# Kernel tuning notes

Measured on AMD Instinct MI355X. Metric: run time of the kernel, lower is better.

The kernel has to match this reference:

```python
import jax, jax.numpy as jnp
import numpy as np

NEG = jnp.float32(-1e30)  # finite stand-in for -inf (grad-safe)
B, T_MAX, K_MAX = 64, 2000, 400
BLANK_LOGPROB = -1.0


def setup_inputs() -> dict:
    key = jax.random.key(0)
    k1, k2, k3, k4 = jax.random.split(key, 4)
    attn = jax.random.normal(k1, (B, 1, T_MAX, K_MAX), jnp.float32)
    attn_logprob = jax.random.normal(k2, (B, 1, T_MAX, K_MAX), jnp.float32)
    in_lens = jax.random.randint(k3, (B,), K_MAX // 2, K_MAX + 1)   # text lengths in [200,400]
    out_lens = jax.random.randint(k4, (B,), T_MAX // 2, T_MAX + 1)  # mel lengths in [1000,2000]
    return {"attn": attn, "in_lens": in_lens, "out_lens": out_lens, "attn_logprob": attn_logprob}


def ctc_alignment_loss(attn_logprob, in_lens, out_lens):
    # attn_logprob: [B, 1, T, K]; targets for sample b are arange(1, in_lens[b]+1), blank=0.
    Bn, _, T, K = attn_logprob.shape
    C = K + 1
    # pad blank class (index 0) with constant blank_logprob, as in F.pad(..., value=blank_logprob)
    lp = jnp.concatenate(
        [jnp.full((Bn, T, 1), BLANK_LOGPROB, attn_logprob.dtype), attn_logprob[:, 0]], axis=-1
    )  # [B, T, C]
    # per-sample log_softmax restricted to classes [0 .. in_len] (original slices :key_len+1 first)
    cls_mask = jnp.arange(C)[None, :] <= in_lens[:, None]          # [B, C]
    lp = jnp.where(cls_mask[:, None, :], lp, NEG)
    lp = jax.nn.log_softmax(lp, axis=-1)                            # [B, T, C]

    # extended CTC state sequence: blank, 1, blank, 2, ..., K, blank  (S = 2K+1)
    S = 2 * K + 1
    s = jnp.arange(S)
    ext = jnp.where(s % 2 == 1, (s + 1) // 2, 0)                    # labels per state
    lp_ext = jnp.take(lp, ext, axis=-1)                             # [B, T, S]
    allow2 = (s % 2 == 1) & (s >= 2)                                # skip-transition allowed (targets have no repeats)

    alpha0 = jnp.full((Bn, S), NEG, lp.dtype)
    alpha0 = alpha0.at[:, 0].set(lp_ext[:, 0, 0]).at[:, 1].set(lp_ext[:, 0, 1])

    def step(alpha, inputs):
        lp_t, t = inputs  # lp_t: [B, S]
        a1 = jnp.concatenate([jnp.full((Bn, 1), NEG, alpha.dtype), alpha[:, :-1]], axis=1)
        a2 = jnp.concatenate([jnp.full((Bn, 2), NEG, alpha.dtype), alpha[:, :-2]], axis=1)
        a2 = jnp.where(allow2[None, :], a2, NEG)
        new = lp_t + jnp.logaddexp(jnp.logaddexp(alpha, a1), a2)
        alpha = jnp.where((t < out_lens)[:, None], new, alpha)      # freeze past each sample's query_len
        return alpha, None

    xs = (lp_ext.transpose(1, 0, 2)[1:], jnp.arange(1, T))
    alpha, _ = jax.lax.scan(step, alpha0, xs)

    idx_last = 2 * in_lens                                           # final blank state per sample
    a_last = jnp.take_along_axis(alpha, idx_last[:, None], axis=1)[:, 0]
    a_prev = jnp.take_along_axis(alpha, (idx_last - 1)[:, None], axis=1)[:, 0]
    ll = jnp.logaddexp(a_last, a_prev)
    # nn.CTCLoss(reduction='mean') with batch 1: divide by target length; zero_infinity -> 0
    loss = jnp.where(ll > 0.5 * NEG, -ll / in_lens.astype(lp.dtype), jnp.zeros((), lp.dtype))
    return jnp.mean(loss)


def reference(attn, in_lens, out_lens, attn_logprob):
    # attn is accepted but unused, matching the original forward signature
    return ctc_alignment_loss(attn_logprob, in_lens, out_lens)
```

## Files before the change

### kernel.cpp

```cpp
#include <hip/hip_runtime.h>
#include <cmath>


#define T_MAXN 2000
#define K_MAXN 400

typedef uint32_t uint4v __attribute__((ext_vector_type(4)));

#define G_BYTES   ((size_t)64 * T_MAXN * K_MAXN * 2)
#define LSE_OFF   G_BYTES
#define LSE_BYTES ((size_t)64 * T_MAXN * 4)
#define ZERO_OFF  (LSE_OFF + LSE_BYTES)
#define LOSS_OFF  (ZERO_OFF + 4096)
#define WS_NEED   (LOSS_OFF + 64 * 4)

__device__ __forceinline__ float dpp_wave_shr1(float x)
{
    int r = __builtin_amdgcn_update_dpp(0, (int)__float_as_uint(x),
                                        0x138 , 0xF, 0xF, true);
    return __uint_as_float((uint32_t)r);
}

template <int CTRL>
__device__ __forceinline__ float dpp_mov(float x)
{
    int r = __builtin_amdgcn_update_dpp(0, (int)__float_as_uint(x),
                                        CTRL, 0xF, 0xF, true);
    return __uint_as_float((uint32_t)r);
}

__global__ __launch_bounds__(256)
void prep_kernel(const float* __restrict__ ap_all,
                 const int* __restrict__ in_lens,
                 const int* __restrict__ out_lens,
                 float* __restrict__ lse_out,
                 _Float16* __restrict__ g_out,
                 float* __restrict__ zerobuf)
{
    const int b    = blockIdx.y;
    const int L    = in_lens[b];
    const int Tn   = out_lens[b];
    const int lane = threadIdx.x & 63;
    const int wid  = blockIdx.x * (blockDim.x >> 6) + (threadIdx.x >> 6);
    const int nw   = gridDim.x * (blockDim.x >> 6);

    if (b == 0 && wid == 0) {
        for (int i = lane; i < 1024; i += 64) zerobuf[i] = 0.0f;
    }

    const float* base = ap_all + (size_t)b * (T_MAXN * K_MAXN);
    _Float16*    gb   = g_out  + (size_t)b * (T_MAXN * K_MAXN);
    const int c0 = lane * 8;
    const int cb = (c0 < 392) ? c0 : 392;

    for (int t = wid; t < Tn; t += nw) {
        const float4* p = reinterpret_cast<const float4*>(base + (size_t)t * K_MAXN + cb);
        float4 x0 = p[0], x1 = p[1];
        float v[8] = {x0.x, x0.y, x0.z, x0.w, x1.x, x1.y, x1.z, x1.w};
        float m = -1.0f;
        #pragma unroll
        for (int j = 0; j < 8; ++j) {
            v[j] = (c0 + j < L) ? v[j] : -1e30f;
            m = fmaxf(m, v[j]);
        }
        #pragma unroll
        for (int off = 32; off; off >>= 1) m = fmaxf(m, __shfl_xor(m, off));
        float s = (lane == 0) ? __expf(-1.0f - m) : 0.0f;
        #pragma unroll
        for (int j = 0; j < 8; ++j) s += __expf(v[j] - m);
        #pragma unroll
        for (int off = 32; off; off >>= 1) s += __shfl_xor(s, off);
        if (lane == 0) lse_out[b * T_MAXN + t] = m + __logf(s);

        _Float16 h[8];
        #pragma unroll
        for (int j = 0; j < 8; ++j) h[j] = (_Float16)__expf(v[j] + 1.0f);
        if (c0 < K_MAXN)
            *reinterpret_cast<uint4v*>(gb + (size_t)t * K_MAXN + c0) =
                *reinterpret_cast<const uint4v*>(h);
    }
}

__global__ __launch_bounds__(256, 1)
void ctc_scan4w_kernel(const char* wsro,
                       const int* __restrict__ in_lens,
                       const int* __restrict__ out_lens,
                       float* loss_out)
{
    __shared__ float afin[1024];
    __shared__ float halo_sh[4][32];
    __shared__ float wmax_sh[4];

    const int b    = blockIdx.x;
    const int tid  = threadIdx.x;
    const int wid  = tid >> 6;
    const int lane = tid & 63;
    const int L    = in_lens[b];
    const int Tn   = out_lens[b];
    const uint32_t goff = (uint32_t)b * (uint32_t)(T_MAXN * K_MAXN * 2);
    const float* lse = (const float*)(wsro + LSE_OFF) + b * T_MAXN;

    const int col0 = 112 * wid - 16 + 2 * lane;
    uint32_t off, inc;
    if (col0 >= 0 && col0 < K_MAXN) { off = goff + (uint32_t)(col0 * 2) + 800u; inc = 3200u; }
    else                            { off = (uint32_t)ZERO_OFF;                 inc = 0u;    }

    float sl = 0.0f;
    if (wid == 0) {
        for (int t = lane; t < Tn; t += 64) sl += lse[t];
        #pragma unroll
        for (int o = 32; o; o >>= 1) sl += __shfl_xor(sl, o);
    }

    float a0=0.0f, a1=0.0f, a2=0.0f, a3=0.0f;
    if (wid == 0 && lane == 8) {
        a0 = 1.0f;
        a1 = (float)*reinterpret_cast<const _Float16*>(wsro + goff);
    }
    int   E  = 0;
    float t1 = 0.0f;

    #define LOADG4(QA, QB, QC, QD) do { \
        asm volatile("global_load_dword %0, %1, %2 offset:0"    : "=v"(QA) : "v"(off), "s"(wsro)); \
        asm volatile("global_load_dword %0, %1, %2 offset:800"  : "=v"(QB) : "v"(off), "s"(wsro)); \
        asm volatile("global_load_dword %0, %1, %2 offset:1600" : "=v"(QC) : "v"(off), "s"(wsro)); \
        asm volatile("global_load_dword %0, %1, %2 offset:2400" : "=v"(QD) : "v"(off), "s"(wsro)); \
        off += inc; \
    } while (0)

    #define WAITG12 do { \
        asm volatile("s_waitcnt vmcnt(12)" ::: "memory"); \
        __builtin_amdgcn_sched_barrier(0); \
    } while (0)

    #define FMIXLO(DST, SRC, O) \
        asm("v_fma_mix_f32 %0, %1, %2, 0 op_sel:[0,0,0] op_sel_hi:[1,0,0]" \
            : "=v"(DST) : "v"(SRC), "v"(O))
    #define FMIXHI(DST, SRC, O) \
        asm("v_fma_mix_f32 %0, %1, %2, 0 op_sel:[1,0,0] op_sel_hi:[1,0,0]" \
            : "=v"(DST) : "v"(SRC), "v"(O))

    #define STEPF(Q) do { \
        const float e0 = a0 + t1; \
        const float e1 = a2 + a1; \
        const float o0 = a1 + e0; \
        const float o1 = a3 + e1; \
        a0 = e0; a2 = e1; \
        FMIXLO(a1, (Q), o0); \
        FMIXHI(a3, (Q), o1); \
        t1 = dpp_wave_shr1(a3); \
    } while (0)

    #define BARR do { \
        asm volatile("s_waitcnt lgkmcnt(0)" ::: "memory"); \
        __builtin_amdgcn_s_barrier(); \
        asm volatile("" ::: "memory"); \
    } while (0)

    #define EXCHANGE do { \
        float mx = fmaxf(fmaxf(a0, a1), fmaxf(a2, a3)); \
        mx = fmaxf(mx, dpp_mov<0x111>(mx)); \
        mx = fmaxf(mx, dpp_mov<0x112>(mx)); \
        mx = fmaxf(mx, dpp_mov<0x114>(mx)); \
        mx = fmaxf(mx, dpp_mov<0x118>(mx)); \
        mx = fmaxf(mx, dpp_mov<0x142>(mx)); \
        mx = fmaxf(mx, dpp_mov<0x143>(mx)); \
        if (lane == 63) wmax_sh[wid] = mx; \
        if (lane >= 56) { \
            float4 bv; bv.x = a0; bv.y = a1; bv.z = a2; bv.w = a3; \
            *reinterpret_cast<float4*>(&halo_sh[wid][(lane - 56) * 4]) = bv; \
        } \
        BARR; \
        float bm = fmaxf(fmaxf(wmax_sh[0], wmax_sh[1]), fmaxf(wmax_sh[2], wmax_sh[3])); \
        int e = (int)((__float_as_uint(bm) >> 23) & 0xFF) - 127; \
        E += e; \
        const float sc = __uint_as_float((uint32_t)(127 - e) << 23);   \
        if (wid > 0 && lane < 8) { \
            float4 hv = *reinterpret_cast<const float4*>(&halo_sh[wid - 1][lane * 4]); \
            a0 = hv.x; a1 = hv.y; a2 = hv.z; a3 = hv.w; \
        } \
        a0 *= sc; a1 *= sc; a2 *= sc; a3 *= sc; \
        t1 = dpp_wave_shr1(a3); \
        BARR; \
    } while (0)

    uint32_t q0,q1,q2,q3,q4,q5,q6,q7,q8,q9,q10,q11,q12,q13,q14,q15;
    LOADG4(q0,q1,q2,q3); LOADG4(q4,q5,q6,q7);
    LOADG4(q8,q9,q10,q11); LOADG4(q12,q13,q14,q15);

    int t = 1;
    while (t + 15 < Tn) {
        WAITG12; STEPF(q0);  STEPF(q1);  STEPF(q2);  STEPF(q3);  LOADG4(q0,q1,q2,q3);
        WAITG12; STEPF(q4);  STEPF(q5);  STEPF(q6);  STEPF(q7);  LOADG4(q4,q5,q6,q7);
        WAITG12; STEPF(q8);  STEPF(q9);  STEPF(q10); STEPF(q11); LOADG4(q8,q9,q10,q11);
        WAITG12; STEPF(q12); STEPF(q13); STEPF(q14); STEPF(q15); LOADG4(q12,q13,q14,q15);
        EXCHANGE;
        t += 16;
    }
    asm volatile("s_waitcnt vmcnt(0)" ::: "memory");
    __builtin_amdgcn_sched_barrier(0);
    {
        const int r = Tn - t;
        if (r > 0)  STEPF(q0);
        if (r > 1)  STEPF(q1);
        if (r > 2)  STEPF(q2);
        if (r > 3)  STEPF(q3);
        if (r > 4)  STEPF(q4);
        if (r > 5)  STEPF(q5);
        if (r > 6)  STEPF(q6);
        if (r > 7)  STEPF(q7);
        if (r > 8)  STEPF(q8);
        if (r > 9)  STEPF(q9);
        if (r > 10) STEPF(q10);
        if (r > 11) STEPF(q11);
        if (r > 12) STEPF(q12);
        if (r > 13) STEPF(q13);
        if (r > 14) STEPF(q14);
    }

    if (lane >= 8) {
        const int gidx = 224 * wid - 32 + 4 * lane;
        afin[gidx]     = a0;
        afin[gidx + 1] = a1;
        afin[gidx + 2] = a2;
        afin[gidx + 3] = a3;
    }
    __syncthreads();
    if (tid == 0) {
        float tot = afin[2 * L] + afin[2 * L - 1];
        float lossb = 0.0f;
        if (tot > 0.0f) {
            double ll = log((double)tot)
                      + (double)E * 0.69314718055994530942
                      + (double)(-(double)Tn - (double)sl);
            lossb = (float)(-ll / (double)L);
        }
        loss_out[b] = lossb;
    }
    #undef STEPF
    #undef FMIXLO
    #undef FMIXHI
    #undef LOADG4
    #undef WAITG12
    #undef BARR
    #undef EXCHANGE
}

__global__ __launch_bounds__(256)
void lse_kernel(const float* __restrict__ ap_all,
                const int* __restrict__ in_lens,
                float* __restrict__ lse_out)
{
    const int lane = threadIdx.x & 63;
    const int wglob = blockIdx.x * (blockDim.x >> 6) + (threadIdx.x >> 6);
    const int nwav = gridDim.x * (blockDim.x >> 6);
    const int nrows = 64 * T_MAXN;

    for (int row = wglob; row < nrows; row += nwav) {
        const int b = row / T_MAXN;
        const int L = in_lens[b];
        const float* rp = ap_all + (size_t)row * K_MAXN;
        const int c0 = lane * 8;
        const int cb = (c0 < 392) ? c0 : 392;
        const float4* p = reinterpret_cast<const float4*>(rp + cb);
        float4 x0 = p[0], x1 = p[1];
        float v[8] = {x0.x, x0.y, x0.z, x0.w, x1.x, x1.y, x1.z, x1.w};
        float m = -1.0f;
        #pragma unroll
        for (int j = 0; j < 8; ++j) {
            v[j] = (c0 + j < L) ? v[j] : -1e30f;
            m = fmaxf(m, v[j]);
        }
        #pragma unroll
        for (int off = 32; off; off >>= 1) m = fmaxf(m, __shfl_xor(m, off));
        float s = (lane == 0) ? __expf(-1.0f - m) : 0.0f;
        #pragma unroll
        for (int j = 0; j < 8; ++j) s += __expf(v[j] - m);
        #pragma unroll
        for (int off = 32; off; off >>= 1) s += __shfl_xor(s, off);
        if (lane == 0) lse_out[row] = m + __logf(s);
    }
}

__global__ __launch_bounds__(64)
void ctc_scan_kernel(const float* __restrict__ ap_all,
                     const int* __restrict__ in_lens,
                     const int* __restrict__ out_lens,
                     const float* __restrict__ lse_all,
                     float* __restrict__ loss_out)
{
    __shared__ float afin[1024];

    const int b    = blockIdx.x;
    const int lane = threadIdx.x;
    const int L    = in_lens[b];
    const int Tn   = out_lens[b];
    const float* ap  = ap_all + (size_t)b * (T_MAXN * K_MAXN);
    const float* lse = lse_all + b * T_MAXN;

    const float LOG2E = 1.4426950408889634f;
    const int c0 = lane * 8;
    const int cb = (c0 < 392) ? c0 : 392;
    const float* rbase = ap + cb;
    float fa0,fa1,fa2,fa3,fa4,fa5,fa6,fa7;
    float fb0,fb1,fb2,fb3,fb4,fb5,fb6,fb7;
    #define MASKC(J, FA, FB) do { bool ok = (c0 + (J)) < L; \
        FA = ok ? LOG2E : 0.0f; FB = ok ? LOG2E : -1000.0f; } while (0)
    MASKC(0,fa0,fb0); MASKC(1,fa1,fb1); MASKC(2,fa2,fb2); MASKC(3,fa3,fb3);
    MASKC(4,fa4,fb4); MASKC(5,fa5,fb5); MASKC(6,fa6,fb6); MASKC(7,fa7,fb7);
    #undef MASKC

    float4 p0a,p0b,p1a,p1b,p2a,p2b,p3a,p3b;
    #define LOADROW(PA, PB, T) do { \
        const float4* _p = reinterpret_cast<const float4*>(rbase + (size_t)(T) * K_MAXN); \
        PA = _p[0]; PB = _p[1]; } while (0)
    LOADROW(p0a,p0b,1); LOADROW(p1a,p1b,2); LOADROW(p2a,p2b,3); LOADROW(p3a,p3b,4);

    float sl = 0.0f;
    for (int t = lane; t < Tn; t += 64) sl += lse[t];
    #pragma unroll
    for (int off = 32; off; off >>= 1) sl += __shfl_xor(sl, off);

    float x00 = ap[0];
    float a0=0,a1=0,a2=0,a3=0,a4=0,a5=0,a6=0,a7=0;
    float a8=0,a9=0,a10=0,a11=0,a12=0,a13=0,a14=0,a15=0;
    if (lane == 0) {
        a0 = 1.0f;
        a1 = __builtin_amdgcn_exp2f(fmaf(x00, LOG2E, LOG2E));
    }
    int E = 0;

    #define STEP(A0, A1) do { \
        float t1 = __shfl_up(a15, 1); \
        t1 = lane ? t1 : 0.0f; \
        const float f0 = __builtin_amdgcn_exp2f(fmaf((A0).x, fa0, fb0)); \
        const float f1 = __builtin_amdgcn_exp2f(fmaf((A0).y, fa1, fb1)); \
        const float f2 = __builtin_amdgcn_exp2f(fmaf((A0).z, fa2, fb2)); \
        const float f3 = __builtin_amdgcn_exp2f(fmaf((A0).w, fa3, fb3)); \
        const float f4 = __builtin_amdgcn_exp2f(fmaf((A1).x, fa4, fb4)); \
        const float f5 = __builtin_amdgcn_exp2f(fmaf((A1).y, fa5, fb5)); \
        const float f6 = __builtin_amdgcn_exp2f(fmaf((A1).z, fa6, fb6)); \
        const float f7 = __builtin_amdgcn_exp2f(fmaf((A1).w, fa7, fb7)); \
        const float e0 = a0 + t1,   e1 = a2 + a1,   e2 = a4 + a3,   e3 = a6 + a5; \
        const float e4 = a8 + a7,   e5 = a10 + a9,  e6 = a12 + a11, e7 = a14 + a13; \
        const float o0 = a1 + e0,   o1 = a3 + e1,   o2 = a5 + e2,   o3 = a7 + e3; \
        const float o4 = a9 + e4,   o5 = a11 + e5,  o6 = a13 + e6,  o7 = a15 + e7; \
        a0 = e0; a2 = e1; a4 = e2; a6 = e3; a8 = e4; a10 = e5; a12 = e6; a14 = e7; \
        a1 = f0*o0; a3 = f1*o1; a5 = f2*o2; a7 = f3*o3; \
        a9 = f4*o4; a11 = f5*o5; a13 = f6*o6; a15 = f7*o7; \
    } while (0)

    #define RESCALE do { \
        float mx = fmaxf(fmaxf(fmaxf(fmaxf(a0,a1),fmaxf(a2,a3)),fmaxf(fmaxf(a4,a5),fmaxf(a6,a7))), \
                         fmaxf(fmaxf(fmaxf(a8,a9),fmaxf(a10,a11)),fmaxf(fmaxf(a12,a13),fmaxf(a14,a15)))); \
        _Pragma("unroll") \
        for (int off = 32; off; off >>= 1) mx = fmaxf(mx, __shfl_xor(mx, off)); \
        int e = (int)((__float_as_uint(mx) >> 23) & 0xFF) - 127; \
        if (e != 0) { \
            E += e; \
            a0 = ldexpf(a0,-e);  a1 = ldexpf(a1,-e);  a2 = ldexpf(a2,-e);  a3 = ldexpf(a3,-e); \
            a4 = ldexpf(a4,-e);  a5 = ldexpf(a5,-e);  a6 = ldexpf(a6,-e);  a7 = ldexpf(a7,-e); \
            a8 = ldexpf(a8,-e);  a9 = ldexpf(a9,-e);  a10= ldexpf(a10,-e); a11= ldexpf(a11,-e); \
            a12= ldexpf(a12,-e); a13= ldexpf(a13,-e); a14= ldexpf(a14,-e); a15= ldexpf(a15,-e); \
        } \
    } while (0)

    int t = 1;
    while (t + 3 < Tn) {
        int tl;
        STEP(p0a,p0b); tl = (t+4 < T_MAXN) ? t+4 : T_MAXN-1; LOADROW(p0a,p0b,tl);
        STEP(p1a,p1b); tl = (t+5 < T_MAXN) ? t+5 : T_MAXN-1; LOADROW(p1a,p1b,tl);
        STEP(p2a,p2b); tl = (t+6 < T_MAXN) ? t+6 : T_MAXN-1; LOADROW(p2a,p2b,tl);
        STEP(p3a,p3b); tl = (t+7 < T_MAXN) ? t+7 : T_MAXN-1; LOADROW(p3a,p3b,tl);
        if ((t & 7) == 5) RESCALE;
        t += 4;
    }
    if (t < Tn) { STEP(p0a,p0b); ++t; }
    if (t < Tn) { STEP(p1a,p1b); ++t; }
    if (t < Tn) { STEP(p2a,p2b); ++t; }

    afin[16*lane+0]=a0;  afin[16*lane+1]=a1;  afin[16*lane+2]=a2;  afin[16*lane+3]=a3;
    afin[16*lane+4]=a4;  afin[16*lane+5]=a5;  afin[16*lane+6]=a6;  afin[16*lane+7]=a7;
    afin[16*lane+8]=a8;  afin[16*lane+9]=a9;  afin[16*lane+10]=a10; afin[16*lane+11]=a11;
    afin[16*lane+12]=a12; afin[16*lane+13]=a13; afin[16*lane+14]=a14; afin[16*lane+15]=a15;
    __syncthreads();
    if (lane == 0) {
        float tot = afin[2*L] + afin[2*L-1];
        float lossb = 0.0f;
        if (tot > 0.0f) {
            double ll = log((double)tot)
                      + (double)E * 0.69314718055994530942
                      + (double)(-(double)Tn - (double)sl);
            lossb = (float)(-ll / (double)L);
        }
        loss_out[b] = lossb;
    }
    #undef STEP
    #undef RESCALE
    #undef LOADROW
}

__global__ void mean_kernel(const float* __restrict__ loss, float* __restrict__ out)
{
    float v = loss[threadIdx.x];
    #pragma unroll
    for (int off = 32; off; off >>= 1) v += __shfl_xor(v, off);
    if (threadIdx.x == 0) out[0] = v * (1.0f / 64.0f);
}

extern "C" void kernel_launch(void* const* d_in, const int* in_sizes, int n_in,
                              void* d_out, int out_size, void* d_ws, size_t ws_size,
                              hipStream_t stream)
{
    const int*   in_lens  = (const int*)d_in[1];
    const int*   out_lens = (const int*)d_in[2];
    const float* ap       = (const float*)d_in[3];
    float*       out      = (float*)d_out;

    if (ws_size >= WS_NEED) {
        char*     wsb     = (char*)d_ws;
        _Float16* g       = (_Float16*)wsb;
        float*    lse_ws  = (float*)(wsb + LSE_OFF);
        float*    zb      = (float*)(wsb + ZERO_OFF);
        float*    loss_ws = (float*)(wsb + LOSS_OFF);
        hipLaunchKernelGGL(prep_kernel, dim3(32, 64), dim3(256), 0, stream,
                           ap, in_lens, out_lens, lse_ws, g, zb);
        hipLaunchKernelGGL(ctc_scan4w_kernel, dim3(64), dim3(256), 0, stream,
                           (const char*)wsb, in_lens, out_lens, loss_ws);
        hipLaunchKernelGGL(mean_kernel, dim3(1), dim3(64), 0, stream, loss_ws, out);
    } else {
        float* lse_ws  = (float*)d_ws;
        float* loss_ws = (float*)((char*)d_ws + (size_t)64 * T_MAXN * 4);
        hipLaunchKernelGGL(lse_kernel, dim3(512), dim3(256), 0, stream,
                           ap, in_lens, lse_ws);
        hipLaunchKernelGGL(ctc_scan_kernel, dim3(64), dim3(64), 0, stream,
                           ap, in_lens, out_lens, lse_ws, loss_ws);
        hipLaunchKernelGGL(mean_kernel, dim3(1), dim3(64), 0, stream, loss_ws, out);
    }
}
```

Before: 120.1 us.

## Double-buffer halo exchange to drop second barrier; use plain C loads

```diff
diff --git a/kernel.cpp b/kernel.cpp
--- a/kernel.cpp
+++ b/kernel.cpp
@@ -88,8 +88,8 @@
                        float* loss_out)
 {
     __shared__ float afin[1024];
-    __shared__ float halo_sh[4][32];
-    __shared__ float wmax_sh[4];
+    __shared__ float halo_sh[2][4][32];
+    __shared__ float wmax_sh[2][4];
 
     const int b    = blockIdx.x;
     const int tid  = threadIdx.x;
@@ -121,16 +121,11 @@
     float t1 = 0.0f;
 
     #define LOADG4(QA, QB, QC, QD) do { \
-        asm volatile("global_load_dword %0, %1, %2 offset:0"    : "=v"(QA) : "v"(off), "s"(wsro)); \
-        asm volatile("global_load_dword %0, %1, %2 offset:800"  : "=v"(QB) : "v"(off), "s"(wsro)); \
-        asm volatile("global_load_dword %0, %1, %2 offset:1600" : "=v"(QC) : "v"(off), "s"(wsro)); \
-        asm volatile("global_load_dword %0, %1, %2 offset:2400" : "=v"(QD) : "v"(off), "s"(wsro)); \
+        QA = *reinterpret_cast<const uint32_t*>(wsro + off); \
+        QB = *reinterpret_cast<const uint32_t*>(wsro + off + 800); \
+        QC = *reinterpret_cast<const uint32_t*>(wsro + off + 1600); \
+        QD = *reinterpret_cast<const uint32_t*>(wsro + off + 2400); \
         off += inc; \
-    } while (0)
-
-    #define WAITG12 do { \
-        asm volatile("s_waitcnt vmcnt(12)" ::: "memory"); \
-        __builtin_amdgcn_sched_barrier(0); \
     } while (0)
 
     #define FMIXLO(DST, SRC, O) \
@@ -157,7 +152,7 @@
         asm volatile("" ::: "memory"); \
     } while (0)
 
-    #define EXCHANGE do { \
+    #define EXCHANGE(PP) do { \
         float mx = fmaxf(fmaxf(a0, a1), fmaxf(a2, a3)); \
         mx = fmaxf(mx, dpp_mov<0x111>(mx)); \
         mx = fmaxf(mx, dpp_mov<0x112>(mx)); \
@@ -165,23 +160,23 @@
         mx = fmaxf(mx, dpp_mov<0x118>(mx)); \
         mx = fmaxf(mx, dpp_mov<0x142>(mx)); \
         mx = fmaxf(mx, dpp_mov<0x143>(mx)); \
-        if (lane == 63) wmax_sh[wid] = mx; \
+        if (lane == 63) wmax_sh[PP][wid] = mx; \
         if (lane >= 56) { \
             float4 bv; bv.x = a0; bv.y = a1; bv.z = a2; bv.w = a3; \
-            *reinterpret_cast<float4*>(&halo_sh[wid][(lane - 56) * 4]) = bv; \
+            *reinterpret_cast<float4*>(&halo_sh[PP][wid][(lane - 56) * 4]) = bv; \
         } \
         BARR; \
-        float bm = fmaxf(fmaxf(wmax_sh[0], wmax_sh[1]), fmaxf(wmax_sh[2], wmax_sh[3])); \
+        float bm = fmaxf(fmaxf(wmax_sh[PP][0], wmax_sh[PP][1]), \
+                         fmaxf(wmax_sh[PP][2], wmax_sh[PP][3])); \
         int e = (int)((__float_as_uint(bm) >> 23) & 0xFF) - 127; \
         E += e; \
         const float sc = __uint_as_float((uint32_t)(127 - e) << 23);   \
         if (wid > 0 && lane < 8) { \
-            float4 hv = *reinterpret_cast<const float4*>(&halo_sh[wid - 1][lane * 4]); \
+            float4 hv = *reinterpret_cast<const float4*>(&halo_sh[PP][wid - 1][lane * 4]); \
             a0 = hv.x; a1 = hv.y; a2 = hv.z; a3 = hv.w; \
         } \
         a0 *= sc; a1 *= sc; a2 *= sc; a3 *= sc; \
         t1 = dpp_wave_shr1(a3); \
-        BARR; \
     } while (0)
 
     uint32_t q0,q1,q2,q3,q4,q5,q6,q7,q8,q9,q10,q11,q12,q13,q14,q15;
@@ -189,16 +184,16 @@
     LOADG4(q8,q9,q10,q11); LOADG4(q12,q13,q14,q15);
 
     int t = 1;
+    int pp = 0;
     while (t + 15 < Tn) {
-        WAITG12; STEPF(q0);  STEPF(q1);  STEPF(q2);  STEPF(q3);  LOADG4(q0,q1,q2,q3);
-        WAITG12; STEPF(q4);  STEPF(q5);  STEPF(q6);  STEPF(q7);  LOADG4(q4,q5,q6,q7);
-        WAITG12; STEPF(q8);  STEPF(q9);  STEPF(q10); STEPF(q11); LOADG4(q8,q9,q10,q11);
-        WAITG12; STEPF(q12); STEPF(q13); STEPF(q14); STEPF(q15); LOADG4(q12,q13,q14,q15);
-        EXCHANGE;
+        STEPF(q0);  STEPF(q1);  STEPF(q2);  STEPF(q3);  LOADG4(q0,q1,q2,q3);
+        STEPF(q4);  STEPF(q5);  STEPF(q6);  STEPF(q7);  LOADG4(q4,q5,q6,q7);
+        STEPF(q8);  STEPF(q9);  STEPF(q10); STEPF(q11); LOADG4(q8,q9,q10,q11);
+        STEPF(q12); STEPF(q13); STEPF(q14); STEPF(q15); LOADG4(q12,q13,q14,q15);
+        EXCHANGE(pp);
+        pp ^= 1;
         t += 16;
     }
-    asm volatile("s_waitcnt vmcnt(0)" ::: "memory");
-    __builtin_amdgcn_sched_barrier(0);
     {
         const int r = Tn - t;
         if (r > 0)  STEPF(q0);
@@ -241,7 +236,6 @@
     #undef FMIXLO
     #undef FMIXHI
     #undef LOADG4
-    #undef WAITG12
     #undef BARR
     #undef EXCHANGE
 }
```

Result: faster. 117.0 us (median of 2 runs) (-2.5%).
